# Kernel optimization log

Hardware: AMD Instinct MI355X
Metric: run time of the kernel (lower is better)

The kernel has to match this reference:

```python
import jax, jax.numpy as jnp
import numpy as np

N, E = 50000, 600000
C_IN, HID, C_OUT = 128, 128, 64


def setup_inputs() -> dict:
    key = jax.random.key(0)
    ks = jax.random.split(key, 8)
    x = jax.random.normal(ks[0], (N, C_IN), dtype=jnp.float32)
    edge_index = jax.random.randint(ks[1], (2, E), 0, N, dtype=jnp.int64)
    s1 = 1.0 / np.sqrt(C_IN)
    s2 = 1.0 / np.sqrt(HID)
    W1 = jax.random.normal(ks[2], (C_IN, HID), dtype=jnp.float32) * s1
    b1 = jnp.zeros((HID,), dtype=jnp.float32)
    W2 = jax.random.normal(ks[3], (HID, HID), dtype=jnp.float32) * s2
    b2 = jnp.zeros((HID,), dtype=jnp.float32)
    Wo = jax.random.normal(ks[4], (HID, C_OUT), dtype=jnp.float32) * s2
    bo = jnp.zeros((C_OUT,), dtype=jnp.float32)
    return {"x": x, "edge_index": edge_index, "W1": W1, "b1": b1,
            "W2": W2, "b2": b2, "Wo": Wo, "bo": bo}


def _gcn_layer(x, src, dst, deg_isqrt, W, b):
    # GCNConv: x' = D^{-1/2} (A + I) D^{-1/2} X W + b, then ReLU
    h = x @ W                                   # [N, out]
    norm = deg_isqrt[src] * deg_isqrt[dst]      # [E+N]
    msg = h[src] * norm[:, None]                # gather + scale
    agg = jax.ops.segment_sum(msg, dst, num_segments=x.shape[0])
    return jax.nn.relu(agg + b)


def reference(x, edge_index, W1, b1, W2, b2, Wo, bo):
    n = x.shape[0]
    loop = jnp.arange(n, dtype=edge_index.dtype)
    src = jnp.concatenate([edge_index[0], loop])  # add self loops
    dst = jnp.concatenate([edge_index[1], loop])
    deg = jax.ops.segment_sum(jnp.ones_like(src, dtype=x.dtype), dst,
                              num_segments=n)
    deg_isqrt = jax.lax.rsqrt(deg)  # deg >= 1 due to self loops
    h = _gcn_layer(x, src, dst, deg_isqrt, W1, b1)
    h = _gcn_layer(h, src, dst, deg_isqrt, W2, b2)
    return h @ Wo + bo
```

## Files before the change

kernel.cpp:

```cpp
#include <hip/hip_runtime.h>


static inline int cdiv_i(long long a, long long b) { return (int)((a + b - 1) / b); }

__device__ __forceinline__ long long load_idx(const void* p, long long i, int is64) {
  return is64 ? ((const long long*)p)[i] : (long long)((const int*)p)[i];
}

__global__ void k_detect(const void* __restrict__ eidx, int* __restrict__ flag) {
  if (blockIdx.x == 0 && threadIdx.x == 0) {
    const unsigned int* p = (const unsigned int*)eidx;
    int is64 = 1;
    for (int i = 0; i < 64; ++i) {
      if (p[2 * i + 1] != 0u) { is64 = 0; break; }
    }
    *flag = is64;
  }
}

__global__ void k_zero2(int* __restrict__ a, int* __restrict__ b, int n) {
  int i = blockIdx.x * 256 + threadIdx.x;
  if (i < n) { a[i] = 0; b[i] = 0; }
}

__global__ void k_hist(const void* __restrict__ eidx, const int* __restrict__ flag,
                       int* __restrict__ counts, int E) {
  int is64 = *flag;
  int e = blockIdx.x * 256 + threadIdx.x;
  if (e < E) {
    long long dst = load_idx(eidx, (long long)E + e, is64);
    atomicAdd(&counts[dst], 1);
  }
}

__global__ void k_disq(const int* __restrict__ counts, float* __restrict__ disq, int n) {
  int i = blockIdx.x * 256 + threadIdx.x;
  if (i < n) disq[i] = rsqrtf(1.0f + (float)counts[i]);
}

__global__ __launch_bounds__(256) void k_scan_local(const int* __restrict__ counts,
                                                    int* __restrict__ offsets,
                                                    int* __restrict__ partials, int n) {
  __shared__ int sd[256];
  int tid = threadIdx.x;
  int i = blockIdx.x * 256 + tid;
  int v = (i < n) ? counts[i] : 0;
  sd[tid] = v;
  __syncthreads();
  for (int off = 1; off < 256; off <<= 1) {
    int t = (tid >= off) ? sd[tid - off] : 0;
    __syncthreads();
    sd[tid] += t;
    __syncthreads();
  }
  if (i < n) offsets[i] = sd[tid] - v;
  if (tid == 255) partials[blockIdx.x] = sd[255];
}

__global__ __launch_bounds__(256) void k_scan_partials(int* __restrict__ partials, int nblk) {
  __shared__ int sd[256];
  __shared__ int carry_s;
  int tid = threadIdx.x;
  if (tid == 0) carry_s = 0;
  __syncthreads();
  for (int base = 0; base < nblk; base += 256) {
    int i = base + tid;
    int v = (i < nblk) ? partials[i] : 0;
    sd[tid] = v;
    __syncthreads();
    for (int off = 1; off < 256; off <<= 1) {
      int t = (tid >= off) ? sd[tid - off] : 0;
      __syncthreads();
      sd[tid] += t;
      __syncthreads();
    }
    int carry = carry_s;
    if (i < nblk) partials[i] = carry + sd[tid] - v;
    __syncthreads();
    if (tid == 0) carry_s = carry + sd[255];
    __syncthreads();
  }
}

__global__ void k_scan_add(int* __restrict__ offsets, const int* __restrict__ partials, int n) {
  int i = blockIdx.x * 256 + threadIdx.x;
  if (i < n) offsets[i] += partials[blockIdx.x];
}

__global__ void k_fill(const void* __restrict__ eidx, const int* __restrict__ flag,
                       const int* __restrict__ offsets, int* __restrict__ cursor,
                       int* __restrict__ csr_src, int E) {
  int is64 = *flag;
  int e = blockIdx.x * 256 + threadIdx.x;
  if (e < E) {
    long long src = load_idx(eidx, e, is64);
    long long dst = load_idx(eidx, (long long)E + e, is64);
    int pos = offsets[dst] + atomicAdd(&cursor[dst], 1);
    csr_src[pos] = (int)src;
  }
}

template <int COLS, int ROWS, bool HIDDEN>
__global__ __launch_bounds__(256, 4) void k_gemm_t(
    const float* __restrict__ X, const float* __restrict__ W,
    const float* __restrict__ disq, const float* __restrict__ bias,
    float* __restrict__ H, int n) {
  constexpr int CT = COLS / 4;
  constexpr int PAD = 4;
  __shared__ float Xs[128][ROWS + PAD];

  const int row0 = blockIdx.x * ROWS;

  {
    constexpr int KT = 256 / ROWS;
    constexpr int NL4 = 32 / KT;
    const int srow = (int)threadIdx.x / KT;
    const int skq = (int)threadIdx.x % KT;
    const int grow = row0 + srow;
    const bool valid = grow < n;
    const float4* xg = (const float4*)(X + (long long)grow * 128);
#pragma unroll
    for (int i = 0; i < NL4; ++i) {
      int k4 = skq + i * KT;
      float4 v = valid ? xg[k4] : make_float4(0.f, 0.f, 0.f, 0.f);
      Xs[k4 * 4 + 0][srow] = v.x;
      Xs[k4 * 4 + 1][srow] = v.y;
      Xs[k4 * 4 + 2][srow] = v.z;
      Xs[k4 * 4 + 3][srow] = v.w;
    }
  }
  __syncthreads();

  const int c0 = ((int)threadIdx.x % CT) * 4;
  const int r0 = ((int)threadIdx.x / CT) * 4;

  float acc[4][4] = {};
#pragma unroll 8
  for (int k = 0; k < 128; ++k) {
    const float4 xr = *(const float4*)&Xs[k][r0];
    const float4 w = *(const float4*)&W[k * COLS + c0];
#pragma unroll
    for (int i = 0; i < 4; ++i) {
      float a = (&xr.x)[i];
      acc[i][0] = fmaf(a, w.x, acc[i][0]);
      acc[i][1] = fmaf(a, w.y, acc[i][1]);
      acc[i][2] = fmaf(a, w.z, acc[i][2]);
      acc[i][3] = fmaf(a, w.w, acc[i][3]);
    }
  }

#pragma unroll
  for (int i = 0; i < 4; ++i) {
    int row = row0 + r0 + i;
    if (row < n) {
      float4 o = make_float4(acc[i][0], acc[i][1], acc[i][2], acc[i][3]);
      if (HIDDEN) {
        float s = disq[row];
        o.x *= s; o.y *= s; o.z *= s; o.w *= s;
      } else {
        const float4 b = *(const float4*)&bias[c0];
        o.x += b.x; o.y += b.y; o.z += b.z; o.w += b.w;
      }
      *(float4*)&H[(long long)row * COLS + c0] = o;
    }
  }
}

__global__ __launch_bounds__(256) void k_aggregate(
    const float* __restrict__ H, const int* __restrict__ csr_src,
    const int* __restrict__ offsets, const int* __restrict__ counts,
    const float* __restrict__ disq, const float* __restrict__ bias,
    float* __restrict__ X2, int n) {
  int dst = blockIdx.x * 4 + ((int)threadIdx.x >> 6);
  if (dst >= n) return;
  int lane = threadIdx.x & 63;
  int c = lane * 2;

  float2 acc = *(const float2*)&H[(long long)dst * 128 + c];
  int beg = offsets[dst];
  int cnt = counts[dst];

  int navail = cnt < 64 ? cnt : 64;
  int myidx = (lane < navail) ? csr_src[beg + lane] : 0;

  int j = 0;
  for (; j + 4 <= navail; j += 4) {
    int s0 = __shfl(myidx, j, 64);
    int s1 = __shfl(myidx, j + 1, 64);
    int s2 = __shfl(myidx, j + 2, 64);
    int s3 = __shfl(myidx, j + 3, 64);
    float2 v0 = *(const float2*)&H[(long long)s0 * 128 + c];
    float2 v1 = *(const float2*)&H[(long long)s1 * 128 + c];
    float2 v2 = *(const float2*)&H[(long long)s2 * 128 + c];
    float2 v3 = *(const float2*)&H[(long long)s3 * 128 + c];
    acc.x += v0.x + v1.x + v2.x + v3.x;
    acc.y += v0.y + v1.y + v2.y + v3.y;
  }
  for (; j < navail; ++j) {
    int s = __shfl(myidx, j, 64);
    float2 v = *(const float2*)&H[(long long)s * 128 + c];
    acc.x += v.x;
    acc.y += v.y;
  }
  for (int jj = beg + 64; jj < beg + cnt; ++jj) {
    int s = csr_src[jj];
    float2 v = *(const float2*)&H[(long long)s * 128 + c];
    acc.x += v.x;
    acc.y += v.y;
  }

  float s = disq[dst];
  float2 b = *(const float2*)&bias[c];
  float2 r;
  r.x = fmaxf(fmaf(s, acc.x, b.x), 0.f);
  r.y = fmaxf(fmaf(s, acc.y, b.y), 0.f);
  *(float2*)&X2[(long long)dst * 128 + c] = r;
}

extern "C" void kernel_launch(void* const* d_in, const int* in_sizes, int n_in,
                              void* d_out, int out_size, void* d_ws, size_t ws_size,
                              hipStream_t stream) {
  (void)n_in; (void)out_size; (void)ws_size;
  const float* x  = (const float*)d_in[0];
  const void*  ei = d_in[1];
  const float* W1 = (const float*)d_in[2];
  const float* b1 = (const float*)d_in[3];
  const float* W2 = (const float*)d_in[4];
  const float* b2 = (const float*)d_in[5];
  const float* Wo = (const float*)d_in[6];
  const float* bo = (const float*)d_in[7];
  float* out = (float*)d_out;

  const int N = in_sizes[0] / 128;
  const int E = in_sizes[1] / 2;
  const int nblk_n = cdiv_i(N, 256);

  char* ws = (char*)d_ws;
  size_t off = 0;
  auto alloc = [&](size_t bytes) {
    void* p = ws + off;
    off += (bytes + 255) & ~(size_t)255;
    return p;
  };
  int*   flag     = (int*)alloc(4);
  int*   counts   = (int*)alloc((size_t)N * 4);
  int*   cursor   = (int*)alloc((size_t)N * 4);
  int*   offsets  = (int*)alloc((size_t)N * 4);
  int*   partials = (int*)alloc((size_t)nblk_n * 4);
  float* disq     = (float*)alloc((size_t)N * 4);
  int*   csr_src  = (int*)alloc((size_t)E * 4);
  float* H        = (float*)alloc((size_t)N * 128 * 4);
  float* X2       = (float*)alloc((size_t)N * 128 * 4);

  k_detect<<<1, 64, 0, stream>>>(ei, flag);
  k_zero2<<<nblk_n, 256, 0, stream>>>(counts, cursor, N);
  k_hist<<<cdiv_i(E, 256), 256, 0, stream>>>(ei, flag, counts, E);
  k_disq<<<nblk_n, 256, 0, stream>>>(counts, disq, N);
  k_scan_local<<<nblk_n, 256, 0, stream>>>(counts, offsets, partials, N);
  k_scan_partials<<<1, 256, 0, stream>>>(partials, nblk_n);
  k_scan_add<<<nblk_n, 256, 0, stream>>>(offsets, partials, N);
  k_fill<<<cdiv_i(E, 256), 256, 0, stream>>>(ei, flag, offsets, cursor, csr_src, E);

  const int agg_blocks = cdiv_i(N, 4);

  k_gemm_t<128, 32, true><<<cdiv_i(N, 32), 256, 0, stream>>>(x, W1, disq, b1, H, N);
  k_aggregate<<<agg_blocks, 256, 0, stream>>>(H, csr_src, offsets, counts, disq, b1, X2, N);
  k_gemm_t<128, 32, true><<<cdiv_i(N, 32), 256, 0, stream>>>(X2, W2, disq, b2, H, N);
  k_aggregate<<<agg_blocks, 256, 0, stream>>>(H, csr_src, offsets, counts, disq, b2, X2, N);
  k_gemm_t<64, 64, false><<<cdiv_i(N, 64), 256, 0, stream>>>(X2, Wo, nullptr, bo, out, N);
}
```

Baseline: 335.7 us.

## Store hidden features as fp16 and enlarge GEMM row tiles

The pre-scaled hidden features H are now written by the GEMM as packed half2 and read by the aggregation kernel as half2. This halves the bytes moved in the gather-heavy aggregation. The GEMM template is also generalised so each thread computes more rows (RPT), doubling rows per block for all three GEMMs to reuse W loads across more rows. The cost is fp16 rounding of intermediate features, which may affect accuracy, plus higher register pressure in the GEMM.

```diff
diff --git a/kernel.cpp b/kernel.cpp
--- a/kernel.cpp
+++ b/kernel.cpp
@@ -1,4 +1,5 @@
 #include <hip/hip_runtime.h>
+#include <hip/hip_fp16.h>
 
 
 static inline int cdiv_i(long long a, long long b) { return (int)((a + b - 1) / b); }
@@ -104,8 +105,10 @@
 __global__ __launch_bounds__(256, 4) void k_gemm_t(
     const float* __restrict__ X, const float* __restrict__ W,
     const float* __restrict__ disq, const float* __restrict__ bias,
-    float* __restrict__ H, int n) {
+    void* __restrict__ OUT, int n) {
   constexpr int CT = COLS / 4;
+  constexpr int RG = 256 / CT;
+  constexpr int RPT = ROWS / RG;
   constexpr int PAD = 4;
   __shared__ float Xs[128][ROWS + PAD];
 
@@ -132,51 +135,57 @@
   __syncthreads();
 
   const int c0 = ((int)threadIdx.x % CT) * 4;
-  const int r0 = ((int)threadIdx.x / CT) * 4;
-
-  float acc[4][4] = {};
-#pragma unroll 8
+  const int r0 = ((int)threadIdx.x / CT) * RPT;
+
+  float acc[RPT][4] = {};
+#pragma unroll 4
   for (int k = 0; k < 128; ++k) {
-    const float4 xr = *(const float4*)&Xs[k][r0];
     const float4 w = *(const float4*)&W[k * COLS + c0];
 #pragma unroll
-    for (int i = 0; i < 4; ++i) {
-      float a = (&xr.x)[i];
-      acc[i][0] = fmaf(a, w.x, acc[i][0]);
-      acc[i][1] = fmaf(a, w.y, acc[i][1]);
-      acc[i][2] = fmaf(a, w.z, acc[i][2]);
-      acc[i][3] = fmaf(a, w.w, acc[i][3]);
-    }
-  }
-
-#pragma unroll
-  for (int i = 0; i < 4; ++i) {
+    for (int j = 0; j < RPT / 4; ++j) {
+      const float4 xr = *(const float4*)&Xs[k][r0 + j * 4];
+#pragma unroll
+      for (int i = 0; i < 4; ++i) {
+        float a = (&xr.x)[i];
+        acc[j * 4 + i][0] = fmaf(a, w.x, acc[j * 4 + i][0]);
+        acc[j * 4 + i][1] = fmaf(a, w.y, acc[j * 4 + i][1]);
+        acc[j * 4 + i][2] = fmaf(a, w.z, acc[j * 4 + i][2]);
+        acc[j * 4 + i][3] = fmaf(a, w.w, acc[j * 4 + i][3]);
+      }
+    }
+  }
+
+#pragma unroll
+  for (int i = 0; i < RPT; ++i) {
     int row = row0 + r0 + i;
     if (row < n) {
-      float4 o = make_float4(acc[i][0], acc[i][1], acc[i][2], acc[i][3]);
       if (HIDDEN) {
         float s = disq[row];
-        o.x *= s; o.y *= s; o.z *= s; o.w *= s;
+        __half2* Hh = (__half2*)OUT;
+        union { __half2 h2[2]; uint2 u; } pk;
+        pk.h2[0] = __floats2half2_rn(acc[i][0] * s, acc[i][1] * s);
+        pk.h2[1] = __floats2half2_rn(acc[i][2] * s, acc[i][3] * s);
+        *(uint2*)&Hh[(long long)row * (COLS / 2) + c0 / 2] = pk.u;
       } else {
         const float4 b = *(const float4*)&bias[c0];
-        o.x += b.x; o.y += b.y; o.z += b.z; o.w += b.w;
+        float4 o = make_float4(acc[i][0] + b.x, acc[i][1] + b.y,
+                               acc[i][2] + b.z, acc[i][3] + b.w);
+        *(float4*)&((float*)OUT)[(long long)row * COLS + c0] = o;
       }
-      *(float4*)&H[(long long)row * COLS + c0] = o;
     }
   }
 }
 
 __global__ __launch_bounds__(256) void k_aggregate(
-    const float* __restrict__ H, const int* __restrict__ csr_src,
+    const __half2* __restrict__ Hh, const int* __restrict__ csr_src,
     const int* __restrict__ offsets, const int* __restrict__ counts,
     const float* __restrict__ disq, const float* __restrict__ bias,
     float* __restrict__ X2, int n) {
   int dst = blockIdx.x * 4 + ((int)threadIdx.x >> 6);
   if (dst >= n) return;
   int lane = threadIdx.x & 63;
-  int c = lane * 2;
-
-  float2 acc = *(const float2*)&H[(long long)dst * 128 + c];
+
+  float2 acc = __half22float2(Hh[(long long)dst * 64 + lane]);
   int beg = offsets[dst];
   int cnt = counts[dst];
 
@@ -189,27 +198,27 @@
     int s1 = __shfl(myidx, j + 1, 64);
     int s2 = __shfl(myidx, j + 2, 64);
     int s3 = __shfl(myidx, j + 3, 64);
-    float2 v0 = *(const float2*)&H[(long long)s0 * 128 + c];
-    float2 v1 = *(const float2*)&H[(long long)s1 * 128 + c];
-    float2 v2 = *(const float2*)&H[(long long)s2 * 128 + c];
-    float2 v3 = *(const float2*)&H[(long long)s3 * 128 + c];
+    float2 v0 = __half22float2(Hh[(long long)s0 * 64 + lane]);
+    float2 v1 = __half22float2(Hh[(long long)s1 * 64 + lane]);
+    float2 v2 = __half22float2(Hh[(long long)s2 * 64 + lane]);
+    float2 v3 = __half22float2(Hh[(long long)s3 * 64 + lane]);
     acc.x += v0.x + v1.x + v2.x + v3.x;
     acc.y += v0.y + v1.y + v2.y + v3.y;
   }
   for (; j < navail; ++j) {
     int s = __shfl(myidx, j, 64);
-    float2 v = *(const float2*)&H[(long long)s * 128 + c];
+    float2 v = __half22float2(Hh[(long long)s * 64 + lane]);
     acc.x += v.x;
     acc.y += v.y;
   }
   for (int jj = beg + 64; jj < beg + cnt; ++jj) {
-    int s = csr_src[jj];
-    float2 v = *(const float2*)&H[(long long)s * 128 + c];
+    float2 v = __half22float2(Hh[(long long)csr_src[jj] * 64 + lane]);
     acc.x += v.x;
     acc.y += v.y;
   }
 
   float s = disq[dst];
+  int c = lane * 2;
   float2 b = *(const float2*)&bias[c];
   float2 r;
   r.x = fmaxf(fmaf(s, acc.x, b.x), 0.f);
@@ -242,15 +251,15 @@
     off += (bytes + 255) & ~(size_t)255;
     return p;
   };
-  int*   flag     = (int*)alloc(4);
-  int*   counts   = (int*)alloc((size_t)N * 4);
-  int*   cursor   = (int*)alloc((size_t)N * 4);
-  int*   offsets  = (int*)alloc((size_t)N * 4);
-  int*   partials = (int*)alloc((size_t)nblk_n * 4);
-  float* disq     = (float*)alloc((size_t)N * 4);
-  int*   csr_src  = (int*)alloc((size_t)E * 4);
-  float* H        = (float*)alloc((size_t)N * 128 * 4);
-  float* X2       = (float*)alloc((size_t)N * 128 * 4);
+  int*     flag     = (int*)alloc(4);
+  int*     counts   = (int*)alloc((size_t)N * 4);
+  int*     cursor   = (int*)alloc((size_t)N * 4);
+  int*     offsets  = (int*)alloc((size_t)N * 4);
+  int*     partials = (int*)alloc((size_t)nblk_n * 4);
+  float*   disq     = (float*)alloc((size_t)N * 4);
+  int*     csr_src  = (int*)alloc((size_t)E * 4);
+  __half2* Hh       = (__half2*)alloc((size_t)N * 64 * 4);
+  float*   X2       = (float*)alloc((size_t)N * 128 * 4);
 
   k_detect<<<1, 64, 0, stream>>>(ei, flag);
   k_zero2<<<nblk_n, 256, 0, stream>>>(counts, cursor, N);
@@ -263,9 +272,9 @@
 
   const int agg_blocks = cdiv_i(N, 4);
 
-  k_gemm_t<128, 32, true><<<cdiv_i(N, 32), 256, 0, stream>>>(x, W1, disq, b1, H, N);
-  k_aggregate<<<agg_blocks, 256, 0, stream>>>(H, csr_src, offsets, counts, disq, b1, X2, N);
-  k_gemm_t<128, 32, true><<<cdiv_i(N, 32), 256, 0, stream>>>(X2, W2, disq, b2, H, N);
-  k_aggregate<<<agg_blocks, 256, 0, stream>>>(H, csr_src, offsets, counts, disq, b2, X2, N);
-  k_gemm_t<64, 64, false><<<cdiv_i(N, 64), 256, 0, stream>>>(X2, Wo, nullptr, bo, out, N);
-}
+  k_gemm_t<128, 64, true><<<cdiv_i(N, 64), 256, 0, stream>>>(x, W1, disq, b1, Hh, N);
+  k_aggregate<<<agg_blocks, 256, 0, stream>>>(Hh, csr_src, offsets, counts, disq, b1, X2, N);
+  k_gemm_t<128, 64, true><<<cdiv_i(N, 64), 256, 0, stream>>>(X2, W2, disq, b2, Hh, N);
+  k_aggregate<<<agg_blocks, 256, 0, stream>>>(Hh, csr_src, offsets, counts, disq, b2, X2, N);
+  k_gemm_t<64, 128, false><<<cdiv_i(N, 128), 256, 0, stream>>>(X2, Wo, nullptr, bo, out, N);
+}
```

Result: faster. 291.1 us (-13.3%).
